# Kernel optimization log

Measured on AMD Instinct MI355X. Metric: run time of the kernel, lower is better.

The kernel has to match this reference:

```python
import jax, jax.numpy as jnp
import numpy as np

S, V, T = 128, 64, 128
N_RBF, CUTOFF = 16, 6.0
N_ATOM, N_PROT, N_FRAG, N_BATCH = 8192, 16384, 1024, 8
K, R, EPS = 32, 3.0, 1e-4
ES_DIM = N_RBF + S + S + T  # 400
HID = 256
GATE = S + 2 * V  # 256


def rbf_encode(d):
    mu = jnp.linspace(0.0, CUTOFF, N_RBF)
    gamma = N_RBF / CUTOFF
    return jnp.exp(-jnp.square(gamma * (d[..., None] - mu)))


def tp_conv(hs, hv, src, dst, diff, es, valid, n_dst, W1, b1, W2, b2, Ws, Wv):
    """Gather -> edge-scalar-gated tensor product -> scatter-add (EquivariantTPConv)."""
    w = jax.nn.silu(es @ W1 + b1) @ W2 + b2                      # [E, S+2V] edge gates
    unit = diff / (jnp.linalg.norm(diff, axis=-1, keepdims=True) + 1e-8)
    xs = hs[src] @ Ws                                            # [E, S]
    xv = jnp.einsum('evc,vw->ewc', hv[src], Wv)                  # [E, V, 3]
    ms = jnp.where(valid[:, None], w[:, :S] * xs, 0.0)
    mv = jnp.where(valid[:, None, None],
                   w[:, S:S + V, None] * xv + w[:, S + V:, None] * unit[:, None, :], 0.0)
    agg_s = jax.ops.segment_sum(ms, dst, num_segments=n_dst)
    agg_v = jax.ops.segment_sum(mv.reshape(-1, V * 3), dst, num_segments=n_dst).reshape(n_dst, V, 3)
    return agg_s, agg_v


def fragment_inertia(local_pos, fragment_id):
    r2 = jnp.sum(local_pos * local_pos, axis=-1)
    eye = jnp.eye(3, dtype=local_pos.dtype)
    I_atom = r2[:, None, None] * eye - local_pos[:, :, None] * local_pos[:, None, :]
    I_frag = jax.ops.segment_sum(I_atom.reshape(-1, 9), fragment_id, num_segments=N_FRAG).reshape(N_FRAG, 3, 3)
    trace = jnp.trace(I_frag, axis1=-2, axis2=-1)[:, None, None]
    return I_frag + EPS * jnp.maximum(trace, 1.0) * eye


def _forward(atom_pos, prot_pos, local_pos, h_atom_s, h_atom_v, h_prot_s, h_prot_v,
             h_frag_s, h_frag_v, t_emb_atom,
             W1_ra, b1_ra, W2_ra, b2_ra, Ws_ra, Wv_ra,
             W1_af, b1_af, W2_af, b2_af, Ws_af, Wv_af,
             Wo_s, Wo_v, Wf_s, Wf_v,
             fragment_id, atom_batch, prot_batch):
    # ---- bipartite radius graph prot -> atom via masked cdist + topk ----
    d2 = (jnp.sum(atom_pos * atom_pos, -1)[:, None]
          + jnp.sum(prot_pos * prot_pos, -1)[None, :]
          - 2.0 * atom_pos @ prot_pos.T)
    dist = jnp.sqrt(jnp.maximum(d2, 0.0))                        # [N_ATOM, N_PROT]
    mask = (dist <= R) & (atom_batch[:, None] == prot_batch[None, :])
    dinf = jnp.where(mask, dist, jnp.inf)
    neg_top, src = jax.lax.top_k(-dinf, K)                       # K nearest per atom
    valid = jnp.isfinite(neg_top).reshape(-1)
    src = src.reshape(-1)
    dst = jnp.repeat(jnp.arange(N_ATOM), K)
    # ---- residue->atom TP conv ----
    diff_ra = atom_pos[dst] - prot_pos[src]
    dist_ra = jnp.linalg.norm(diff_ra, axis=-1)
    ra_es = jnp.concatenate([rbf_encode(dist_ra), h_prot_s[src], h_atom_s[dst], t_emb_atom[dst]], -1)
    ms, mv = tp_conv(h_prot_s, h_prot_v, src, dst, diff_ra, ra_es, valid, N_ATOM,
                     W1_ra, b1_ra, W2_ra, b2_ra, Ws_ra, Wv_ra)
    ha_s = h_atom_s + jax.nn.silu(ms @ Wo_s)
    ha_v = h_atom_v + jnp.einsum('nvc,vw->nwc', mv, Wo_v)
    # ---- fragment centers + atom->frag re-lift TP conv ----
    ones = jnp.ones((N_ATOM,), atom_pos.dtype)
    cnt = jnp.maximum(jax.ops.segment_sum(ones, fragment_id, num_segments=N_FRAG), 1.0)
    T_frag = jax.ops.segment_sum(atom_pos, fragment_id, num_segments=N_FRAG) / cnt[:, None]
    r_af = atom_pos - T_frag[fragment_id]
    af_es = jnp.concatenate([rbf_encode(jnp.linalg.norm(r_af, axis=-1)), ha_s,
                             h_frag_s[fragment_id], t_emb_atom], -1)
    af_valid = jnp.ones((N_ATOM,), bool)
    fs, fv = tp_conv(ha_s, ha_v, jnp.arange(N_ATOM), fragment_id, r_af, af_es, af_valid, N_FRAG,
                     W1_af, b1_af, W2_af, b2_af, Ws_af, Wv_af)
    hf_s = h_frag_s + jax.nn.silu(fs @ Wf_s)
    hf_v = h_frag_v + jnp.einsum('nvc,vw->nwc', fv, Wf_v)
    I_frag = fragment_inertia(local_pos, fragment_id)
    # single packed output [N_ATOM, 2*(S+3V)+9]; frag quantities gathered per atom
    return jnp.concatenate([ha_s, ha_v.reshape(N_ATOM, -1),
                            hf_s[fragment_id], hf_v.reshape(N_FRAG, -1)[fragment_id],
                            I_frag.reshape(N_FRAG, 9)[fragment_id]], -1)


def setup_inputs() -> dict:
    key = jax.random.key(0)
    ks = jax.random.split(key, 32)
    def w(k, shape, fan_in):
        return jax.random.normal(k, shape, jnp.float32) / np.sqrt(fan_in).astype(np.float32)
    return dict(
        atom_pos=jax.random.normal(ks[0], (N_ATOM, 3), jnp.float32),
        prot_pos=jax.random.normal(ks[1], (N_PROT, 3), jnp.float32),
        local_pos=jax.random.normal(ks[2], (N_ATOM, 3), jnp.float32),
        h_atom_s=jax.random.normal(ks[3], (N_ATOM, S), jnp.float32),
        h_atom_v=jax.random.normal(ks[4], (N_ATOM, V, 3), jnp.float32),
        h_prot_s=jax.random.normal(ks[5], (N_PROT, S), jnp.float32),
        h_prot_v=jax.random.normal(ks[6], (N_PROT, V, 3), jnp.float32),
        h_frag_s=jax.random.normal(ks[7], (N_FRAG, S), jnp.float32),
        h_frag_v=jax.random.normal(ks[8], (N_FRAG, V, 3), jnp.float32),
        t_emb_atom=jax.random.normal(ks[9], (N_ATOM, T), jnp.float32),
        W1_ra=w(ks[10], (ES_DIM, HID), ES_DIM), b1_ra=jnp.zeros((HID,), jnp.float32),
        W2_ra=w(ks[11], (HID, GATE), HID), b2_ra=jnp.zeros((GATE,), jnp.float32),
        Ws_ra=w(ks[12], (S, S), S), Wv_ra=w(ks[13], (V, V), V),
        W1_af=w(ks[14], (ES_DIM, HID), ES_DIM), b1_af=jnp.zeros((HID,), jnp.float32),
        W2_af=w(ks[15], (HID, GATE), HID), b2_af=jnp.zeros((GATE,), jnp.float32),
        Ws_af=w(ks[16], (S, S), S), Wv_af=w(ks[17], (V, V), V),
        Wo_s=w(ks[18], (S, S), S), Wo_v=w(ks[19], (V, V), V),
        Wf_s=w(ks[20], (S, S), S), Wf_v=w(ks[21], (V, V), V),
        fragment_id=jax.random.randint(ks[22], (N_ATOM,), 0, N_FRAG),
        atom_batch=jnp.sort(jax.random.randint(ks[23], (N_ATOM,), 0, N_BATCH)),
        prot_batch=jnp.sort(jax.random.randint(ks[24], (N_PROT,), 0, N_BATCH)),
    )


def reference(atom_pos, prot_pos, local_pos, h_atom_s, h_atom_v, h_prot_s, h_prot_v,
              h_frag_s, h_frag_v, t_emb_atom,
              W1_ra, b1_ra, W2_ra, b2_ra, Ws_ra, Wv_ra,
              W1_af, b1_af, W2_af, b2_af, Ws_af, Wv_af,
              Wo_s, Wo_v, Wf_s, Wf_v,
              fragment_id, atom_batch, prot_batch):
    return _forward(atom_pos, prot_pos, local_pos, h_atom_s, h_atom_v, h_prot_s, h_prot_v,
                    h_frag_s, h_frag_v, t_emb_atom,
                    W1_ra, b1_ra, W2_ra, b2_ra, Ws_ra, Wv_ra,
                    W1_af, b1_af, W2_af, b2_af, Ws_af, Wv_af,
                    Wo_s, Wo_v, Wf_s, Wf_v,
                    fragment_id, atom_batch, prot_batch)
```

## Files before the change

kernel.cpp:

```cpp
#include <hip/hip_runtime.h>
#include <hip/hip_bf16.h>

#define N_ATOM 8192
#define N_PROT 16384
#define N_FRAG 1024
#define KNN    32
#define OUTC   649

typedef __attribute__((ext_vector_type(8))) short bf16x8;
typedef __attribute__((ext_vector_type(4))) float f32x4;

__device__ __forceinline__ float silu_f(float x){ return x / (1.f + __expf(-x)); }
__device__ __forceinline__ unsigned long long ullmin2(unsigned long long a, unsigned long long b){ return a < b ? a : b; }

__device__ __forceinline__ short f2bf(float x){
    __hip_bfloat16 h = __float2bfloat16(x);
    return *reinterpret_cast<short*>(&h);
}
__device__ __forceinline__ unsigned f2bf2(float lo, float hi){
    __hip_bfloat162 h2;
    h2.x = __float2bfloat16(lo);
    h2.y = __float2bfloat16(hi);
    return *reinterpret_cast<unsigned*>(&h2);
}
__device__ __forceinline__ float bf2f(short s){
    return __uint_as_float(((unsigned)(unsigned short)s) << 16);
}

__global__ void k_ranges(const int* __restrict__ pbatch, int* __restrict__ pstart){
    int b = threadIdx.x;
    if (b <= 8){
        int lo = 0, hi = N_PROT;
        while (lo < hi){ int mid = (lo + hi) >> 1; if (pbatch[mid] < b) lo = mid + 1; else hi = mid; }
        pstart[b] = lo;
    }
}

__global__ __launch_bounds__(256) void k_knn(const float* __restrict__ apos,
                                             const float* __restrict__ ppos,
                                             const int* __restrict__ abatch,
                                             const int* __restrict__ pstart,
                                             int* __restrict__ src_out){
    __shared__ int h1[256];
    __shared__ int s_info[4];
    __shared__ int s_nsel;
    __shared__ int s_nbound;
    __shared__ unsigned long long s_bound[512];

    const int i = blockIdx.x, t = threadIdx.x;
    const int lane = t & 63;
    const int b = abatch[i];
    const int p0 = pstart[b], p1 = pstart[b+1];
    const float ax = apos[i*3+0], ay = apos[i*3+1], az = apos[i*3+2];
    const float a2 = ax*ax + ay*ay + az*az;
    const float BINSCALE = 256.0f / 9.0f;

    unsigned kb[12];
    int jj[12];
    int bn[12];
#pragma unroll
    for (int q = 0; q < 12; ++q){
        int j = p0 + q*256 + t;
        unsigned kk = 0xFFFFFFFFu;
        int bin = -1;
        if (j < p1){
            float px = ppos[j*3+0], py = ppos[j*3+1], pz = ppos[j*3+2];
            float p2 = px*px + py*py + pz*pz;
            float dt = ax*px + ay*py + az*pz;
            float d2 = fmaxf((a2 + p2) - 2.0f*dt, 0.f);
            if (d2 <= 9.0f){
                kk = __float_as_uint(d2);
                bin = (int)(d2 * BINSCALE);
                if (bin > 255) bin = 255;
            }
        }
        kb[q] = kk; jj[q] = j; bn[q] = bin;
    }
    h1[t] = 0;
    if (t == 0){ s_nsel = 0; s_nbound = 0; }
    __syncthreads();
#pragma unroll
    for (int q = 0; q < 12; ++q)
        if (bn[q] >= 0) atomicAdd(&h1[bn[q]], 1);
    __syncthreads();
    if (t < 64){
        int base = t*4;
        int a0 = h1[base], a1 = h1[base+1], a2i = h1[base+2], a3 = h1[base+3];
        int lsum = a0 + a1 + a2i + a3;
        int sc = lsum;
#pragma unroll
        for (int off = 1; off < 64; off <<= 1){
            int v = __shfl_up(sc, off);
            if (lane >= off) sc += v;
        }
        int ex = sc - lsum;
        h1[base]   = ex + a0;
        h1[base+1] = ex + a0 + a1;
        h1[base+2] = ex + a0 + a1 + a2i;
        h1[base+3] = sc;
        if (t == 63) s_info[3] = sc;
    }
    __syncthreads();
    const int total = s_info[3];
    const int kth = (total < KNN) ? total : KNN;
    if (kth > 0){
        int cum  = h1[t];
        int prev = (t == 0) ? 0 : h1[t-1];
        if (cum >= kth && prev < kth){ s_info[0] = t; }
    }
    __syncthreads();
    const int B = s_info[0];
    if (kth > 0){
#pragma unroll
        for (int q = 0; q < 12; ++q){
            if (bn[q] < 0) continue;
            if (bn[q] < B){
                int pos = atomicAdd(&s_nsel, 1);
                src_out[i*KNN + pos] = jj[q];
            } else if (bn[q] == B){
                int bi = atomicAdd(&s_nbound, 1);
                if (bi < 512) s_bound[bi] = ((unsigned long long)kb[q] << 32) | (unsigned)jj[q];
            }
        }
    }
    __syncthreads();
    const int base_n = s_nsel;
    const int R = kth - base_n;
    if (t < 64 && R > 0){
        int L = s_nbound; if (L > 512) L = 512;
        for (int r = 0; r < R; ++r){
            unsigned long long m = ~0ull;
            for (int idx = lane; idx < L; idx += 64) m = ullmin2(m, s_bound[idx]);
#pragma unroll
            for (int off = 32; off >= 1; off >>= 1)
                m = ullmin2(m, (unsigned long long)__shfl_xor((unsigned long long)m, off));
            if (lane == 0) src_out[i*KNN + base_n + r] = (int)(unsigned)(m & 0xFFFFFFFFull);
            for (int idx = lane; idx < L; idx += 64)
                if (s_bound[idx] == m) s_bound[idx] = ~0ull;
        }
    }
    if (t < KNN && t >= kth) src_out[i*KNN + t] = -1;
}

__global__ void k_fragsum(const float* __restrict__ apos, const float* __restrict__ lpos,
                          const int* __restrict__ fid,
                          float* __restrict__ cnt, float* __restrict__ tsum, float* __restrict__ isum){
    int a = blockIdx.x*256 + threadIdx.x;
    if (a >= N_ATOM) return;
    int f = fid[a];
    atomicAdd(&cnt[f], 1.f);
    atomicAdd(&tsum[f*3+0], apos[a*3+0]);
    atomicAdd(&tsum[f*3+1], apos[a*3+1]);
    atomicAdd(&tsum[f*3+2], apos[a*3+2]);
    float x = lpos[a*3+0], y = lpos[a*3+1], z = lpos[a*3+2];
    float r2 = x*x + y*y + z*z;
    atomicAdd(&isum[f*9+0], r2 - x*x);
    atomicAdd(&isum[f*9+1], -(x*y));
    atomicAdd(&isum[f*9+2], -(x*z));
    atomicAdd(&isum[f*9+3], -(y*x));
    atomicAdd(&isum[f*9+4], r2 - y*y);
    atomicAdd(&isum[f*9+5], -(y*z));
    atomicAdd(&isum[f*9+6], -(z*x));
    atomicAdd(&isum[f*9+7], -(z*y));
    atomicAdd(&isum[f*9+8], r2 - z*z);
}

__global__ void k_fragcent(const float* __restrict__ cnt, const float* __restrict__ tsum,
                           const float* __restrict__ isum,
                           float* __restrict__ tfrag, float* __restrict__ ifin){
    int f = blockIdx.x*256 + threadIdx.x;
    if (f >= N_FRAG) return;
    float cn = fmaxf(cnt[f], 1.f);
    tfrag[f*3+0] = tsum[f*3+0] / cn;
    tfrag[f*3+1] = tsum[f*3+1] / cn;
    tfrag[f*3+2] = tsum[f*3+2] / cn;
    float tr  = isum[f*9+0] + isum[f*9+4] + isum[f*9+8];
    float add = 1e-4f * fmaxf(tr, 1.f);
#pragma unroll
    for (int q = 0; q < 9; ++q){
        float v = isum[f*9+q];
        if (q == 0 || q == 4 || q == 8) v += add;
        ifin[f*9+q] = v;
    }
}

__global__ __launch_bounds__(1024) void k_csr_prefix(const float* __restrict__ cnt,
                                                     int* __restrict__ csr_off,
                                                     int* __restrict__ csr_cur){
    __shared__ int s[1024];
    int t = threadIdx.x;
    int v = (int)cnt[t];
    s[t] = v;
    __syncthreads();
    for (int off = 1; off < 1024; off <<= 1){
        int x = (t >= off) ? s[t-off] : 0;
        __syncthreads();
        s[t] += x;
        __syncthreads();
    }
    int incl = s[t];
    int excl = incl - v;
    csr_off[t] = excl;
    csr_cur[t] = excl;
    if (t == 1023) csr_off[1024] = incl;
}

__global__ void k_csr_scatter(const int* __restrict__ fid, int* __restrict__ csr_cur,
                              int* __restrict__ csr_atom){
    int a = blockIdx.x*256 + threadIdx.x;
    if (a >= N_ATOM) return;
    int f = fid[a];
    int pos = atomicAdd(&csr_cur[f], 1);
    csr_atom[pos] = a;
}

__global__ void k_pack(const float* __restrict__ W1, const float* __restrict__ W2,
                       const float* __restrict__ Ws, const float* __restrict__ Wv,
                       const float* __restrict__ W1a, const float* __restrict__ W2a,
                       const float* __restrict__ Wsa, const float* __restrict__ Wva,
                       const float* __restrict__ Wos, const float* __restrict__ Wov,
                       short* __restrict__ W1p, short* __restrict__ W2p,
                       short* __restrict__ Wsp, short* __restrict__ Wvp,
                       short* __restrict__ W1cp,
                       short* __restrict__ W1ap, short* __restrict__ W2ap,
                       short* __restrict__ Wsap, short* __restrict__ Wvap,
                       short* __restrict__ Wosp, short* __restrict__ Wovp){
    int id = blockIdx.x*256 + threadIdx.x;
    if (id < 5120){
        int kt = id/1024, rem = id%1024, nt = rem/64, l = rem%64;
#pragma unroll
        for (int jj = 0; jj < 8; ++jj){
            int k = kt*32 + ((l>>4)<<3) + jj, n = nt*16 + (l&15);
            W1p[(size_t)id*8 + jj] = (k < 144) ? f2bf(W1[(size_t)k*256 + n]) : (short)0;
        }
    } else if (id < 13312){
        int id2 = id - 5120;
        int kt = id2/1024, rem = id2%1024, nt = rem/64, l = rem%64;
#pragma unroll
        for (int jj = 0; jj < 8; ++jj){
            int k = kt*32 + ((l>>4)<<3) + jj, n = nt*16 + (l&15);
            W2p[(size_t)id2*8 + jj] = f2bf(W2[(size_t)k*256 + n]);
        }
    } else if (id < 15360){
        int id2 = id - 13312;
        int kt = id2/512, rem = id2%512, nt = rem/64, l = rem%64;
#pragma unroll
        for (int jj = 0; jj < 8; ++jj){
            int k = kt*32 + ((l>>4)<<3) + jj, n = nt*16 + (l&15);
            Wsp[(size_t)id2*8 + jj] = f2bf(Ws[(size_t)k*128 + n]);
        }
    } else if (id < 15872){
        int id2 = id - 15360;
        int kt = id2/256, rem = id2%256, nt = rem/64, l = rem%64;
#pragma unroll
        for (int jj = 0; jj < 8; ++jj){
            int k = kt*32 + ((l>>4)<<3) + jj, n = nt*16 + (l&15);
            Wvp[(size_t)id2*8 + jj] = f2bf(Wv[(size_t)k*64 + n]);
        }
    } else if (id < 24064){
        int id2 = id - 15872;
        int kt = id2/1024, rem = id2%1024, nt = rem/64, l = rem%64;
#pragma unroll
        for (int jj = 0; jj < 8; ++jj){
            int k = kt*32 + ((l>>4)<<3) + jj, n = nt*16 + (l&15);
            W1cp[(size_t)id2*8 + jj] = f2bf(W1[(size_t)(144 + k)*256 + n]);
        }
    } else if (id < 37376){
        int id2 = id - 24064;
        int kt = id2/1024, rem = id2%1024, nt = rem/64, l = rem%64;
#pragma unroll
        for (int jj = 0; jj < 8; ++jj){
            int k = kt*32 + ((l>>4)<<3) + jj, n = nt*16 + (l&15);
            W1ap[(size_t)id2*8 + jj] = (k < 400) ? f2bf(W1a[(size_t)k*256 + n]) : (short)0;
        }
    } else if (id < 45568){
        int id2 = id - 37376;
        int kt = id2/1024, rem = id2%1024, nt = rem/64, l = rem%64;
#pragma unroll
        for (int jj = 0; jj < 8; ++jj){
            int k = kt*32 + ((l>>4)<<3) + jj, n = nt*16 + (l&15);
            W2ap[(size_t)id2*8 + jj] = f2bf(W2a[(size_t)k*256 + n]);
        }
    } else if (id < 47616){
        int id2 = id - 45568;
        int kt = id2/512, rem = id2%512, nt = rem/64, l = rem%64;
#pragma unroll
        for (int jj = 0; jj < 8; ++jj){
            int k = kt*32 + ((l>>4)<<3) + jj, n = nt*16 + (l&15);
            Wsap[(size_t)id2*8 + jj] = f2bf(Wsa[(size_t)k*128 + n]);
        }
    } else if (id < 48128){
        int id2 = id - 47616;
        int kt = id2/256, rem = id2%256, nt = rem/64, l = rem%64;
#pragma unroll
        for (int jj = 0; jj < 8; ++jj){
            int k = kt*32 + ((l>>4)<<3) + jj, n = nt*16 + (l&15);
            Wvap[(size_t)id2*8 + jj] = f2bf(Wva[(size_t)k*64 + n]);
        }
    } else if (id < 50176){
        int id2 = id - 48128;
        int kt = id2/512, rem = id2%512, nt = rem/64, l = rem%64;
#pragma unroll
        for (int jj = 0; jj < 8; ++jj){
            int k = kt*32 + ((l>>4)<<3) + jj, n = nt*16 + (l&15);
            Wosp[(size_t)id2*8 + jj] = f2bf(Wos[(size_t)k*128 + n]);
        }
    } else if (id < 50688){
        int id2 = id - 50176;
        int kt = id2/256, rem = id2%256, nt = rem/64, l = rem%64;
#pragma unroll
        for (int jj = 0; jj < 8; ++jj){
            int k = kt*32 + ((l>>4)<<3) + jj, n = nt*16 + (l&15);
            Wovp[(size_t)id2*8 + jj] = f2bf(Wov[(size_t)k*64 + n]);
        }
    }
}

__global__ __launch_bounds__(256) void k_ctx(const float* __restrict__ has_,
                                             const float* __restrict__ temb,
                                             const short* __restrict__ W1cp,
                                             const float* __restrict__ b1,
                                             float* __restrict__ common){
    __shared__ __align__(16) char s_a[64*512];
    const int t = threadIdx.x, l = t & 63, w = t >> 6, g = l >> 4;
    const int a0 = blockIdx.x * 64;
    {
        int r = t & 63, seg = t >> 6;
        const float* srcp = (seg < 2) ? (has_ + (size_t)(a0 + r)*128 + seg*64)
                                      : (temb + (size_t)(a0 + r)*128 + (seg - 2)*64);
#pragma unroll
        for (int q = 0; q < 16; ++q){
            float4 x = *(const float4*)(srcp + q*4);
            int col = seg*64 + q*4;
            int off = (r*512 + col*2) ^ ((r & 7) << 4);
            *(unsigned*)(s_a + off)     = f2bf2(x.x, x.y);
            *(unsigned*)(s_a + off + 4) = f2bf2(x.z, x.w);
        }
    }
    __syncthreads();
    f32x4 acc[4][4];
#pragma unroll
    for (int mt = 0; mt < 4; ++mt)
#pragma unroll
        for (int nt = 0; nt < 4; ++nt) acc[mt][nt] = (f32x4){0.f,0.f,0.f,0.f};
    for (int ks = 0; ks < 8; ++ks){
        bf16x8 afr[4];
#pragma unroll
        for (int mt = 0; mt < 4; ++mt){
            int row = mt*16 + (l & 15);
            int off = (row*512 + ks*64 + g*16) ^ ((row & 7) << 4);
            afr[mt] = *(const bf16x8*)(s_a + off);
        }
#pragma unroll
        for (int nt = 0; nt < 4; ++nt){
            bf16x8 b = *(const bf16x8*)(W1cp + ((size_t)((ks*16 + (w*4 + nt))*64 + l))*8);
#pragma unroll
            for (int mt = 0; mt < 4; ++mt)
                acc[mt][nt] = __builtin_amdgcn_mfma_f32_16x16x32_bf16(afr[mt], b, acc[mt][nt], 0, 0, 0);
        }
    }
#pragma unroll
    for (int nt = 0; nt < 4; ++nt){
        int col = w*64 + nt*16 + (l & 15);
        float bb = b1[col];
#pragma unroll
        for (int mt = 0; mt < 4; ++mt)
#pragma unroll
            for (int r = 0; r < 4; ++r){
                int row = mt*16 + g*4 + r;
                common[(size_t)(a0 + row)*256 + col] = acc[mt][nt][r] + bb;
            }
    }
}

#define ES_STR 336
__global__ __launch_bounds__(512, 2) void k_ra3(
    const float* __restrict__ apos, const float* __restrict__ ppos,
    const float* __restrict__ hps,  const float* __restrict__ hpv,
    const short* __restrict__ W1p, const short* __restrict__ W2p,
    const short* __restrict__ Wsp, const short* __restrict__ Wvp,
    const float* __restrict__ common, const float* __restrict__ b2,
    const int* __restrict__ src,
    short* __restrict__ msR, short* __restrict__ mvR)
{
    __shared__ __align__(16) char s_es[32*ES_STR];
    __shared__ __align__(16) char s_h1[32*512];
    __shared__ __align__(16) char s_hpv[3*4096];
    __shared__ float s_unit[32][3];

    const int t = threadIdx.x;
    const int i = blockIdx.x;
    const int l = t & 63, w = t >> 6, g = l >> 4, r0 = l & 15;
    const int xm = (r0 & 7) << 4;
    float* s_mvA = (float*)s_es;
    float* s_mvB = s_mvA + 192;

    {
        const int e = t >> 4, sub = t & 15;
        const int j = src[i*KNN + e];
        float dx = 0.f, dy = 0.f, dz = 0.f, dist = 0.f;
        if (j >= 0){
            dx = apos[i*3+0] - ppos[j*3+0];
            dy = apos[i*3+1] - ppos[j*3+1];
            dz = apos[i*3+2] - ppos[j*3+2];
            dist = sqrtf(dx*dx + dy*dy + dz*dz);
        }
        if (sub == 0){
            float inv = 1.f / (dist + 1e-8f);
            s_unit[e][0] = dx*inv; s_unit[e][1] = dy*inv; s_unit[e][2] = dz*inv;
        }
        if (sub < 2){
            const float gamma = 16.0f / 6.0f;
#pragma unroll
            for (int q = 0; q < 4; ++q){
                int kk = sub*8 + q*2;
                float mu0  = 0.4f * (float)kk;
                float mu1  = 0.4f * (float)(kk+1);
                float a0 = gamma * (dist - mu0);
                float a1 = gamma * (dist - mu1);
                float e0 = (j >= 0) ? __expf(-(a0*a0)) : 0.f;
                float e1 = (j >= 0) ? __expf(-(a1*a1)) : 0.f;
                *(unsigned*)(s_es + e*ES_STR + kk*2) = f2bf2(e0, e1);
            }
        }
        if (sub < 8) *(int*)(s_es + e*ES_STR + 288 + sub*4) = 0;
#pragma unroll
        for (int q = 0; q < 2; ++q){
            float4 x = (j >= 0) ? *(const float4*)(hps + (size_t)j*128 + sub*8 + q*4)
                                : make_float4(0.f,0.f,0.f,0.f);
            *(unsigned*)(s_es + e*ES_STR + 32 + sub*16 + q*8)     = f2bf2(x.x, x.y);
            *(unsigned*)(s_es + e*ES_STR + 32 + sub*16 + q*8 + 4) = f2bf2(x.z, x.w);
        }
        const int em = (e & 7) << 4;
#pragma unroll
        for (int q = 0; q < 3; ++q){
            float4 x = (j >= 0) ? *(const float4*)(hpv + (size_t)j*192 + sub*12 + q*4)
                                : make_float4(0.f,0.f,0.f,0.f);
            float xv4[4] = {x.x, x.y, x.z, x.w};
#pragma unroll
            for (int m = 0; m < 4; ++m){
                int idx = sub*12 + q*4 + m;
                int v = idx/3, c = idx - v*3;
                *(short*)(s_hpv + c*4096 + e*128 + ((v*2) ^ em)) = f2bf(xv4[m]);
            }
        }
    }
    __syncthreads();

    f32x4 acc1[2][2];
#pragma unroll
    for (int mt = 0; mt < 2; ++mt)
#pragma unroll
        for (int nt = 0; nt < 2; ++nt) acc1[mt][nt] = (f32x4){0.f,0.f,0.f,0.f};
    for (int ks = 0; ks < 5; ++ks){
        bf16x8 a0 = *(const bf16x8*)(s_es + r0*ES_STR + ks*64 + g*16);
        bf16x8 a1 = *(const bf16x8*)(s_es + (16 + r0)*ES_STR + ks*64 + g*16);
#pragma unroll
        for (int nt = 0; nt < 2; ++nt){
            bf16x8 b = *(const bf16x8*)(W1p + ((size_t)((ks*16 + (w*2 + nt))*64 + l))*8);
            acc1[0][nt] = __builtin_amdgcn_mfma_f32_16x16x32_bf16(a0, b, acc1[0][nt], 0, 0, 0);
            acc1[1][nt] = __builtin_amdgcn_mfma_f32_16x16x32_bf16(a1, b, acc1[1][nt], 0, 0, 0);
        }
    }

#pragma unroll
    for (int nt = 0; nt < 2; ++nt){
        int col = w*32 + nt*16 + r0;
        float cm = common[(size_t)i*256 + col];
#pragma unroll
        for (int mt = 0; mt < 2; ++mt)
#pragma unroll
            for (int r = 0; r < 4; ++r){
                float v = silu_f(acc1[mt][nt][r] + cm);
                int row = mt*16 + g*4 + r;
                int off = (row*512 + col*2) ^ ((row & 7) << 4);
                *(short*)(s_h1 + off) = f2bf(v);
            }
    }

    f32x4 accxs[2][2];
#pragma unroll
    for (int mt = 0; mt < 2; ++mt)
#pragma unroll
        for (int nt = 0; nt < 2; ++nt) accxs[mt][nt] = (f32x4){0.f,0.f,0.f,0.f};
    if (w < 4){
        for (int ks = 0; ks < 4; ++ks){
            bf16x8 a0 = *(const bf16x8*)(s_es + r0*ES_STR + 32 + ks*64 + g*16);
            bf16x8 a1 = *(const bf16x8*)(s_es + (16 + r0)*ES_STR + 32 + ks*64 + g*16);
#pragma unroll
            for (int nt = 0; nt < 2; ++nt){
                bf16x8 b = *(const bf16x8*)(Wsp + ((size_t)((ks*8 + (w*2 + nt))*64 + l))*8);
                accxs[0][nt] = __builtin_amdgcn_mfma_f32_16x16x32_bf16(a0, b, accxs[0][nt], 0, 0, 0);
                accxs[1][nt] = __builtin_amdgcn_mfma_f32_16x16x32_bf16(a1, b, accxs[1][nt], 0, 0, 0);
            }
        }
    }
    __syncthreads();

    f32x4 accw[2][2];
#pragma unroll
    for (int mt = 0; mt < 2; ++mt)
#pragma unroll
        for (int nt = 0; nt < 2; ++nt) accw[mt][nt] = (f32x4){0.f,0.f,0.f,0.f};
    for (int ks = 0; ks < 8; ++ks){
        int off0 = (r0*512 + ks*64 + g*16) ^ xm;
        bf16x8 a0 = *(const bf16x8*)(s_h1 + off0);
        bf16x8 a1 = *(const bf16x8*)(s_h1 + off0 + 8192);
#pragma unroll
        for (int nt = 0; nt < 2; ++nt){
            bf16x8 b = *(const bf16x8*)(W2p + ((size_t)((ks*16 + (w*2 + nt))*64 + l))*8);
            accw[0][nt] = __builtin_amdgcn_mfma_f32_16x16x32_bf16(a0, b, accw[0][nt], 0, 0, 0);
            accw[1][nt] = __builtin_amdgcn_mfma_f32_16x16x32_bf16(a1, b, accw[1][nt], 0, 0, 0);
        }
    }
    float b2v[2];
#pragma unroll
    for (int nt = 0; nt < 2; ++nt) b2v[nt] = b2[w*32 + nt*16 + r0];

    if (w < 4){
#pragma unroll
        for (int nt = 0; nt < 2; ++nt){
            float p = 0.f;
#pragma unroll
            for (int mt = 0; mt < 2; ++mt)
#pragma unroll
                for (int r = 0; r < 4; ++r)
                    p = fmaf(accw[mt][nt][r] + b2v[nt], accxs[mt][nt][r], p);
            p += __shfl_xor(p, 16);
            p += __shfl_xor(p, 32);
            if (l < 16) msR[(size_t)i*128 + w*32 + nt*16 + r0] = f2bf(p);
        }
    } else if (w < 6){
        bf16x8 bv[2][2];
#pragma unroll
        for (int ks = 0; ks < 2; ++ks)
#pragma unroll
            for (int nt = 0; nt < 2; ++nt)
                bv[ks][nt] = *(const bf16x8*)(Wvp + ((size_t)((ks*4 + (w-4)*2 + nt)*64 + l))*8);
#pragma unroll
        for (int c = 0; c < 3; ++c){
            f32x4 accxv[2][2];
#pragma unroll
            for (int mt = 0; mt < 2; ++mt)
#pragma unroll
                for (int nt = 0; nt < 2; ++nt) accxv[mt][nt] = (f32x4){0.f,0.f,0.f,0.f};
#pragma unroll
            for (int ks = 0; ks < 2; ++ks){
                int off0 = c*4096 + r0*128 + ((ks*64 + g*16) ^ xm);
                bf16x8 a0 = *(const bf16x8*)(s_hpv + off0);
                bf16x8 a1 = *(const bf16x8*)(s_hpv + off0 + 2048);
#pragma unroll
                for (int nt = 0; nt < 2; ++nt){
                    accxv[0][nt] = __builtin_amdgcn_mfma_f32_16x16x32_bf16(a0, bv[ks][nt], accxv[0][nt], 0, 0, 0);
                    accxv[1][nt] = __builtin_amdgcn_mfma_f32_16x16x32_bf16(a1, bv[ks][nt], accxv[1][nt], 0, 0, 0);
                }
            }
#pragma unroll
            for (int nt = 0; nt < 2; ++nt){
                float p = 0.f;
#pragma unroll
                for (int mt = 0; mt < 2; ++mt)
#pragma unroll
                    for (int r = 0; r < 4; ++r)
                        p = fmaf(accw[mt][nt][r] + b2v[nt], accxv[mt][nt][r], p);
                p += __shfl_xor(p, 16);
                p += __shfl_xor(p, 32);
                if (l < 16) s_mvA[c*64 + (w-4)*32 + nt*16 + r0] = p;
            }
        }
    } else {
        float uu[8][3];
#pragma unroll
        for (int mt = 0; mt < 2; ++mt)
#pragma unroll
            for (int r = 0; r < 4; ++r){
                int e = mt*16 + g*4 + r;
#pragma unroll
                for (int c = 0; c < 3; ++c) uu[mt*4+r][c] = s_unit[e][c];
            }
#pragma unroll
        for (int c = 0; c < 3; ++c)
#pragma unroll
            for (int nt = 0; nt < 2; ++nt){
                float p = 0.f;
#pragma unroll
                for (int mt = 0; mt < 2; ++mt)
#pragma unroll
                    for (int r = 0; r < 4; ++r)
                        p = fmaf(accw[mt][nt][r] + b2v[nt], uu[mt*4+r][c], p);
                p += __shfl_xor(p, 16);
                p += __shfl_xor(p, 32);
                if (l < 16) s_mvB[c*64 + (w-6)*32 + nt*16 + r0] = p;
            }
    }
    __syncthreads();

    if (t < 192){
        int wi = t & 63, cc = t >> 6;
        float v = s_mvA[cc*64 + wi] + s_mvB[cc*64 + wi];
        mvR[((size_t)i*3 + cc)*64 + wi] = f2bf(v);
    }
}

__global__ __launch_bounds__(256) void k_ra_out(
    const short* __restrict__ msR, const short* __restrict__ mvR,
    const short* __restrict__ Wosp, const short* __restrict__ Wovp,
    const float* __restrict__ has_, const float* __restrict__ hav,
    float* __restrict__ out)
{
    const int t = threadIdx.x, l = t & 63, w = t >> 6, g = l >> 4, r0 = l & 15;
    const int a0 = blockIdx.x * 32;

    f32x4 acc[2][2];
#pragma unroll
    for (int mt = 0; mt < 2; ++mt)
#pragma unroll
        for (int nt = 0; nt < 2; ++nt) acc[mt][nt] = (f32x4){0.f,0.f,0.f,0.f};
    for (int ks = 0; ks < 4; ++ks){
        bf16x8 af0 = *(const bf16x8*)(msR + ((size_t)(a0 + r0)*128 + ks*32 + g*8));
        bf16x8 af1 = *(const bf16x8*)(msR + ((size_t)(a0 + 16 + r0)*128 + ks*32 + g*8));
#pragma unroll
        for (int nt = 0; nt < 2; ++nt){
            bf16x8 b = *(const bf16x8*)(Wosp + ((size_t)((ks*8 + (w*2 + nt))*64 + l))*8);
            acc[0][nt] = __builtin_amdgcn_mfma_f32_16x16x32_bf16(af0, b, acc[0][nt], 0, 0, 0);
            acc[1][nt] = __builtin_amdgcn_mfma_f32_16x16x32_bf16(af1, b, acc[1][nt], 0, 0, 0);
        }
    }
#pragma unroll
    for (int nt = 0; nt < 2; ++nt){
        int col = w*32 + nt*16 + r0;
#pragma unroll
        for (int mt = 0; mt < 2; ++mt)
#pragma unroll
            for (int r = 0; r < 4; ++r){
                int a = a0 + mt*16 + g*4 + r;
                out[(size_t)a*OUTC + col] = has_[(size_t)a*128 + col] + silu_f(acc[mt][nt][r]);
            }
    }

    f32x4 accv[6];
#pragma unroll
    for (int mt = 0; mt < 6; ++mt) accv[mt] = (f32x4){0.f,0.f,0.f,0.f};
    for (int ks = 0; ks < 2; ++ks){
        bf16x8 b = *(const bf16x8*)(Wovp + ((size_t)((ks*4 + w)*64 + l))*8);
#pragma unroll
        for (int mt = 0; mt < 6; ++mt){
            bf16x8 af = *(const bf16x8*)(mvR + ((size_t)(a0*3 + mt*16 + r0)*64 + ks*32 + g*8));
            accv[mt] = __builtin_amdgcn_mfma_f32_16x16x32_bf16(af, b, accv[mt], 0, 0, 0);
        }
    }
    const int wi = w*16 + r0;
#pragma unroll
    for (int mt = 0; mt < 6; ++mt)
#pragma unroll
        for (int r = 0; r < 4; ++r){
            int R = mt*16 + g*4 + r;
            int a = a0 + R/3, c = R - (R/3)*3;
            out[(size_t)a*OUTC + 128 + wi*3 + c] = hav[(size_t)a*192 + wi*3 + c] + accv[mt][r];
        }
}

#define AES_STR 848
__global__ __launch_bounds__(256, 2) void k_af2(
    const float* __restrict__ apos, const float* __restrict__ tfrag,
    const float* __restrict__ hfs_in, const float* __restrict__ temb,
    const short* __restrict__ W1p, const float* __restrict__ b1,
    const short* __restrict__ W2p, const float* __restrict__ b2,
    const short* __restrict__ Wsp, const short* __restrict__ Wvp,
    const int* __restrict__ fragid, const float* __restrict__ out,
    short* __restrict__ msA, short* __restrict__ mvA)
{
    __shared__ __align__(16) char s_es[16*AES_STR];
    __shared__ __align__(16) char s_h1[16*512];
    __shared__ __align__(16) char s_pv[3*2048];
    __shared__ float s_unit[16][3];
    float* s_upr = (float*)s_es;

    const int t = threadIdx.x, a0 = blockIdx.x*16;
    const int l = t & 63, w = t >> 6, g = l >> 4, r0 = l & 15;
    const int xm = (r0 & 7) << 4;

    {
        const int e = t >> 4, sub = t & 15;
        const int a = a0 + e;
        const int f = fragid[a];
        float rx = apos[a*3+0] - tfrag[f*3+0];
        float ry = apos[a*3+1] - tfrag[f*3+1];
        float rz = apos[a*3+2] - tfrag[f*3+2];
        float dist = sqrtf(rx*rx + ry*ry + rz*rz);
        if (sub == 0){
            float inv = 1.f / (dist + 1e-8f);
            s_unit[e][0] = rx*inv; s_unit[e][1] = ry*inv; s_unit[e][2] = rz*inv;
        }
        if (sub < 2){
            const float gamma = 16.0f / 6.0f;
#pragma unroll
            for (int q = 0; q < 4; ++q){
                int kk = sub*8 + q*2;
                float mu0  = 0.4f * (float)kk;
                float mu1  = 0.4f * (float)(kk+1);
                float a0f = gamma * (dist - mu0);
                float a1f = gamma * (dist - mu1);
                *(unsigned*)(s_es + e*AES_STR + kk*2) = f2bf2(__expf(-(a0f*a0f)), __expf(-(a1f*a1f)));
            }
        }
#pragma unroll
        for (int q = 0; q < 4; ++q){
            float v0 = out[(size_t)a*OUTC + sub*8 + q*2];
            float v1 = out[(size_t)a*OUTC + sub*8 + q*2 + 1];
            *(unsigned*)(s_es + e*AES_STR + 32 + (sub*8 + q*2)*2) = f2bf2(v0, v1);
        }
#pragma unroll
        for (int q = 0; q < 2; ++q){
            float4 x = *(const float4*)(hfs_in + (size_t)f*128 + sub*8 + q*4);
            *(unsigned*)(s_es + e*AES_STR + 288 + sub*16 + q*8)     = f2bf2(x.x, x.y);
            *(unsigned*)(s_es + e*AES_STR + 288 + sub*16 + q*8 + 4) = f2bf2(x.z, x.w);
        }
#pragma unroll
        for (int q = 0; q < 2; ++q){
            float4 x = *(const float4*)(temb + (size_t)a*128 + sub*8 + q*4);
            *(unsigned*)(s_es + e*AES_STR + 544 + sub*16 + q*8)     = f2bf2(x.x, x.y);
            *(unsigned*)(s_es + e*AES_STR + 544 + sub*16 + q*8 + 4) = f2bf2(x.z, x.w);
        }
        *(short*)(s_es + e*AES_STR + 800 + sub*2) = 0;
        const int em = (e & 7) << 4;
#pragma unroll
        for (int q = 0; q < 12; ++q){
            int idx = sub*12 + q;
            float v = out[(size_t)a*OUTC + 128 + idx];
            int vv = idx/3, c = idx - vv*3;
            *(short*)(s_pv + c*2048 + e*128 + ((vv*2) ^ em)) = f2bf(v);
        }
    }
    __syncthreads();

    f32x4 acc1[4];
#pragma unroll
    for (int nt = 0; nt < 4; ++nt) acc1[nt] = (f32x4){0.f,0.f,0.f,0.f};
    for (int ks = 0; ks < 13; ++ks){
        bf16x8 a0f = *(const bf16x8*)(s_es + r0*AES_STR + ks*64 + g*16);
#pragma unroll
        for (int nt = 0; nt < 4; ++nt){
            bf16x8 b = *(const bf16x8*)(W1p + ((size_t)((ks*16 + (w*4 + nt))*64 + l))*8);
            acc1[nt] = __builtin_amdgcn_mfma_f32_16x16x32_bf16(a0f, b, acc1[nt], 0, 0, 0);
        }
    }
#pragma unroll
    for (int nt = 0; nt < 4; ++nt){
        int col = w*64 + nt*16 + r0;
        float bb = b1[col];
#pragma unroll
        for (int r = 0; r < 4; ++r){
            float v = silu_f(acc1[nt][r] + bb);
            int row = g*4 + r;
            int off = (row*512 + col*2) ^ ((row & 7) << 4);
            *(short*)(s_h1 + off) = f2bf(v);
        }
    }
    f32x4 accxs[4];
#pragma unroll
    for (int nt = 0; nt < 4; ++nt) accxs[nt] = (f32x4){0.f,0.f,0.f,0.f};
    if (w < 2){
        for (int ks = 0; ks < 4; ++ks){
            bf16x8 a0f = *(const bf16x8*)(s_es + r0*AES_STR + 32 + ks*64 + g*16);
#pragma unroll
            for (int nt = 0; nt < 4; ++nt){
                bf16x8 b = *(const bf16x8*)(Wsp + ((size_t)((ks*8 + (w*4 + nt))*64 + l))*8);
                accxs[nt] = __builtin_amdgcn_mfma_f32_16x16x32_bf16(a0f, b, accxs[nt], 0, 0, 0);
            }
        }
    }
    __syncthreads();

    f32x4 accw[4];
#pragma unroll
    for (int nt = 0; nt < 4; ++nt) accw[nt] = (f32x4){0.f,0.f,0.f,0.f};
    for (int ks = 0; ks < 8; ++ks){
        int off0 = (r0*512 + ks*64 + g*16) ^ xm;
        bf16x8 a0f = *(const bf16x8*)(s_h1 + off0);
#pragma unroll
        for (int nt = 0; nt < 4; ++nt){
            bf16x8 b = *(const bf16x8*)(W2p + ((size_t)((ks*16 + (w*4 + nt))*64 + l))*8);
            accw[nt] = __builtin_amdgcn_mfma_f32_16x16x32_bf16(a0f, b, accw[nt], 0, 0, 0);
        }
    }
    float b2v[4];
#pragma unroll
    for (int nt = 0; nt < 4; ++nt) b2v[nt] = b2[w*64 + nt*16 + r0];

    if (w == 3){
        float uu[4][3];
#pragma unroll
        for (int r = 0; r < 4; ++r){
            int e = g*4 + r;
#pragma unroll
            for (int c = 0; c < 3; ++c) uu[r][c] = s_unit[e][c];
        }
#pragma unroll
        for (int nt = 0; nt < 4; ++nt){
            int wi = nt*16 + r0;
#pragma unroll
            for (int r = 0; r < 4; ++r){
                int e = g*4 + r;
                float gate = accw[nt][r] + b2v[nt];
#pragma unroll
                for (int c = 0; c < 3; ++c)
                    s_upr[e*192 + wi*3 + c] = gate * uu[r][c];
            }
        }
    }
    __syncthreads();

    if (w < 2){
#pragma unroll
        for (int nt = 0; nt < 4; ++nt){
            int col = w*64 + nt*16 + r0;
#pragma unroll
            for (int r = 0; r < 4; ++r){
                int e = g*4 + r;
                float p = (accw[nt][r] + b2v[nt]) * accxs[nt][r];
                msA[(size_t)(a0 + e)*128 + col] = f2bf(p);
            }
        }
    } else if (w == 2){
        bf16x8 bv[2][4];
#pragma unroll
        for (int ks = 0; ks < 2; ++ks)
#pragma unroll
            for (int nt = 0; nt < 4; ++nt)
                bv[ks][nt] = *(const bf16x8*)(Wvp + ((size_t)((ks*4 + nt)*64 + l))*8);
#pragma unroll
        for (int c = 0; c < 3; ++c){
            f32x4 accxv[4];
#pragma unroll
            for (int nt = 0; nt < 4; ++nt) accxv[nt] = (f32x4){0.f,0.f,0.f,0.f};
#pragma unroll
            for (int ks = 0; ks < 2; ++ks){
                int off0 = c*2048 + r0*128 + ((ks*64 + g*16) ^ xm);
                bf16x8 a0f = *(const bf16x8*)(s_pv + off0);
#pragma unroll
                for (int nt = 0; nt < 4; ++nt)
                    accxv[nt] = __builtin_amdgcn_mfma_f32_16x16x32_bf16(a0f, bv[ks][nt], accxv[nt], 0, 0, 0);
            }
#pragma unroll
            for (int nt = 0; nt < 4; ++nt){
                int wi = nt*16 + r0;
#pragma unroll
                for (int r = 0; r < 4; ++r){
                    int e = g*4 + r;
                    float p = (accw[nt][r] + b2v[nt]) * accxv[nt][r]
                            + s_upr[e*192 + wi*3 + c];
                    mvA[(size_t)(a0 + e)*192 + wi*3 + c] = f2bf(p);
                }
            }
        }
    }
}

__global__ __launch_bounds__(256) void k_fragupd(
    const int* __restrict__ csr_off, const int* __restrict__ csr_atom,
    const short* __restrict__ msA, const short* __restrict__ mvA,
    const float* __restrict__ hfs_in, const float* __restrict__ hfv_in,
    const float* __restrict__ Wfs, const float* __restrict__ Wfv,
    const float* __restrict__ ifin,
    float* __restrict__ out)
{
    __shared__ __align__(16) float s_fs[128];
    __shared__ __align__(16) float s_fv[192];
    const int f = blockIdx.x, t = threadIdx.x;
    const int n0 = csr_off[f], n1 = csr_off[f+1];
    if (t < 128){
        float s = 0.f;
        for (int n = n0; n < n1; ++n){
            int a = csr_atom[n];
            s += bf2f(msA[(size_t)a*128 + t]);
        }
        s_fs[t] = s;
    }
    if (t >= 64){
        int idx = t - 64;
        float s = 0.f;
        for (int n = n0; n < n1; ++n){
            int a = csr_atom[n];
            s += bf2f(mvA[(size_t)a*192 + idx]);
        }
        s_fv[(idx % 3)*64 + (idx / 3)] = s;
    }
    __syncthreads();
    if (t < 128){
        float o = 0.f;
        for (int k = 0; k < 128; k += 4){
            const float* wr = &Wfs[k*128 + t];
            float4 m4 = *(const float4*)&s_fs[k];
            o = fmaf(m4.x, wr[0],   o);
            o = fmaf(m4.y, wr[128], o);
            o = fmaf(m4.z, wr[256], o);
            o = fmaf(m4.w, wr[384], o);
        }
        float val = hfs_in[f*128 + t] + silu_f(o);
        for (int n = n0; n < n1; ++n)
            out[(size_t)csr_atom[n]*OUTC + 320 + t] = val;
    }
    if (t < 192){
        const int wi = t & 63, cc = t >> 6;
        float o = 0.f;
        for (int v = 0; v < 64; v += 4){
            const float* wr = &Wfv[v*64 + wi];
            float4 m4 = *(const float4*)&s_fv[cc*64 + v];
            o = fmaf(m4.x, wr[0],   o);
            o = fmaf(m4.y, wr[64],  o);
            o = fmaf(m4.z, wr[128], o);
            o = fmaf(m4.w, wr[192], o);
        }
        float val = hfv_in[f*192 + wi*3 + cc] + o;
        for (int n = n0; n < n1; ++n)
            out[(size_t)csr_atom[n]*OUTC + 448 + wi*3 + cc] = val;
    } else if (t < 201){
        int q = t - 192;
        float val = ifin[f*9 + q];
        for (int n = n0; n < n1; ++n)
            out[(size_t)csr_atom[n]*OUTC + 640 + q] = val;
    }
}

extern "C" void kernel_launch(void* const* d_in, const int* in_sizes, int n_in,
                              void* d_out, int out_size, void* d_ws, size_t ws_size,
                              hipStream_t stream)
{
    const float* atom_pos   = (const float*)d_in[0];
    const float* prot_pos   = (const float*)d_in[1];
    const float* local_pos  = (const float*)d_in[2];
    const float* h_atom_s   = (const float*)d_in[3];
    const float* h_atom_v   = (const float*)d_in[4];
    const float* h_prot_s   = (const float*)d_in[5];
    const float* h_prot_v   = (const float*)d_in[6];
    const float* h_frag_s   = (const float*)d_in[7];
    const float* h_frag_v   = (const float*)d_in[8];
    const float* t_emb      = (const float*)d_in[9];
    const float* W1_ra = (const float*)d_in[10]; const float* b1_ra = (const float*)d_in[11];
    const float* W2_ra = (const float*)d_in[12]; const float* b2_ra = (const float*)d_in[13];
    const float* Ws_ra = (const float*)d_in[14]; const float* Wv_ra = (const float*)d_in[15];
    const float* W1_af = (const float*)d_in[16]; const float* b1_af = (const float*)d_in[17];
    const float* W2_af = (const float*)d_in[18]; const float* b2_af = (const float*)d_in[19];
    const float* Ws_af = (const float*)d_in[20]; const float* Wv_af = (const float*)d_in[21];
    const float* Wo_s  = (const float*)d_in[22]; const float* Wo_v  = (const float*)d_in[23];
    const float* Wf_s  = (const float*)d_in[24]; const float* Wf_v  = (const float*)d_in[25];
    const int* fragment_id = (const int*)d_in[26];
    const int* atom_batch  = (const int*)d_in[27];
    const int* prot_batch  = (const int*)d_in[28];
    float* out = (float*)d_out;

    float* cnt   = (float*)d_ws;
    float* tsum  = cnt  + 1024;
    float* isum  = tsum + 3072;
    float* tfrag = isum + 9216;
    float* ifin  = tfrag + 3072;
    float* hfs   = ifin + 9216;
    float* hfv   = hfs  + 1024*128;
    int*   pstart   = (int*)(hfv + 1024*192);
    int*   src      = pstart + 16;
    int*   csr_off  = src + N_ATOM*KNN;
    int*   csr_cur  = csr_off + 1025;
    int*   csr_atom = csr_cur + 1024;
    uintptr_t pal = ((uintptr_t)(csr_atom + 8192) + 127) & ~(uintptr_t)127;
    float* common = (float*)pal;
    short* msA = (short*)common;
    short* mvA = msA + (size_t)8192*128;
    short* W1p  = (short*)(common + (size_t)8192*256);
    short* W2p  = W1p  + 40960;
    short* Wsp  = W2p  + 65536;
    short* Wvp  = Wsp  + 16384;
    short* W1cp = Wvp  + 4096;
    short* W1ap = W1cp + 65536;
    short* W2ap = W1ap + 106496;
    short* Wsap = W2ap + 65536;
    short* Wvap = Wsap + 16384;
    short* Wosp = Wvap + 4096;
    short* Wovp = Wosp + 16384;
    short* msR  = Wovp + 4096;
    short* mvR  = msR + (size_t)8192*128;

    size_t zero_bytes = (size_t)(1024 + 3072 + 9216) * sizeof(float);
    hipMemsetAsync(cnt, 0, zero_bytes, stream);

    k_pack    <<<198, 256, 0, stream>>>(W1_ra, W2_ra, Ws_ra, Wv_ra, W1_af, W2_af, Ws_af, Wv_af,
                                        Wo_s, Wo_v,
                                        W1p, W2p, Wsp, Wvp, W1cp, W1ap, W2ap, Wsap, Wvap,
                                        Wosp, Wovp);
    k_ranges  <<<1, 64, 0, stream>>>(prot_batch, pstart);
    k_knn     <<<N_ATOM, 256, 0, stream>>>(atom_pos, prot_pos, atom_batch, pstart, src);
    k_ctx     <<<N_ATOM/64, 256, 0, stream>>>(h_atom_s, t_emb, W1cp, b1_ra, common);
    k_fragsum <<<N_ATOM/256, 256, 0, stream>>>(atom_pos, local_pos, fragment_id, cnt, tsum, isum);
    k_fragcent<<<N_FRAG/256, 256, 0, stream>>>(cnt, tsum, isum, tfrag, ifin);
    k_csr_prefix<<<1, 1024, 0, stream>>>(cnt, csr_off, csr_cur);
    k_csr_scatter<<<N_ATOM/256, 256, 0, stream>>>(fragment_id, csr_cur, csr_atom);
    k_ra3     <<<N_ATOM, 512, 0, stream>>>(atom_pos, prot_pos, h_prot_s, h_prot_v,
                                           W1p, W2p, Wsp, Wvp, common, b2_ra,
                                           src, msR, mvR);
    k_ra_out  <<<N_ATOM/32, 256, 0, stream>>>(msR, mvR, Wosp, Wovp, h_atom_s, h_atom_v, out);
    k_af2     <<<N_ATOM/16, 256, 0, stream>>>(atom_pos, tfrag, h_frag_s, t_emb,
                                              W1ap, b1_af, W2ap, b2_af, Wsap, Wvap,
                                              fragment_id, out, msA, mvA);
    k_fragupd <<<N_FRAG, 256, 0, stream>>>(csr_off, csr_atom, msA, mvA,
                                           h_frag_s, h_frag_v, Wf_s, Wf_v, ifin, out);
}
```

Baseline: 252.6 us.

## Pre-convert protein features to bf16 and fold fragcent into CSR prefix kernel

Adds a conversion kernel that turns protein scalar features into bf16 and protein vector features into a channel-major bf16 layout once, instead of converting them for every gathered edge. The radius-graph message kernel then gathers 16-byte bf16 vectors straight into shared memory, which halves gather bytes and removes per-element conversion and scattered short stores. The fragment centroid/inertia finalization is merged into the single-block prefix kernel to save a launch. This costs an extra pass over all protein features and some scratch memory.

```diff
diff --git a/kernel.cpp b/kernel.cpp
--- a/kernel.cpp
+++ b/kernel.cpp
@@ -33,6 +33,33 @@
         int lo = 0, hi = N_PROT;
         while (lo < hi){ int mid = (lo + hi) >> 1; if (pbatch[mid] < b) lo = mid + 1; else hi = mid; }
         pstart[b] = lo;
+    }
+}
+
+__global__ __launch_bounds__(256) void k_cvt(const float* __restrict__ hps,
+                                             const float* __restrict__ hpv,
+                                             short* __restrict__ hpsB,
+                                             short* __restrict__ hpvT){
+    int id = blockIdx.x*256 + threadIdx.x;
+    if (id < N_PROT*16){
+        const float* s = hps + (size_t)id*8;
+        float4 x0 = *(const float4*)(s);
+        float4 x1 = *(const float4*)(s+4);
+        unsigned* d = (unsigned*)(hpsB + (size_t)id*8);
+        d[0] = f2bf2(x0.x, x0.y); d[1] = f2bf2(x0.z, x0.w);
+        d[2] = f2bf2(x1.x, x1.y); d[3] = f2bf2(x1.z, x1.w);
+    } else {
+        int id2 = id - N_PROT*16;
+        if (id2 < N_PROT*24){
+            int j = id2 / 24, r = id2 % 24;
+            short tmp[8];
+#pragma unroll
+            for (int u = 0; u < 8; ++u){
+                int o = r*8 + u, c = o >> 6, v = o & 63;
+                tmp[u] = f2bf(hpv[(size_t)j*192 + v*3 + c]);
+            }
+            *(bf16x8*)(hpvT + (size_t)j*192 + r*8) = *(bf16x8*)tmp;
+        }
     }
 }
 
@@ -165,32 +192,32 @@
     atomicAdd(&isum[f*9+8], r2 - z*z);
 }
 
-__global__ void k_fragcent(const float* __restrict__ cnt, const float* __restrict__ tsum,
-                           const float* __restrict__ isum,
-                           float* __restrict__ tfrag, float* __restrict__ ifin){
-    int f = blockIdx.x*256 + threadIdx.x;
-    if (f >= N_FRAG) return;
-    float cn = fmaxf(cnt[f], 1.f);
-    tfrag[f*3+0] = tsum[f*3+0] / cn;
-    tfrag[f*3+1] = tsum[f*3+1] / cn;
-    tfrag[f*3+2] = tsum[f*3+2] / cn;
-    float tr  = isum[f*9+0] + isum[f*9+4] + isum[f*9+8];
-    float add = 1e-4f * fmaxf(tr, 1.f);
-#pragma unroll
-    for (int q = 0; q < 9; ++q){
-        float v = isum[f*9+q];
-        if (q == 0 || q == 4 || q == 8) v += add;
-        ifin[f*9+q] = v;
-    }
-}
-
 __global__ __launch_bounds__(1024) void k_csr_prefix(const float* __restrict__ cnt,
+                                                     const float* __restrict__ tsum,
+                                                     const float* __restrict__ isum,
                                                      int* __restrict__ csr_off,
-                                                     int* __restrict__ csr_cur){
+                                                     int* __restrict__ csr_cur,
+                                                     float* __restrict__ tfrag,
+                                                     float* __restrict__ ifin){
     __shared__ int s[1024];
     int t = threadIdx.x;
-    int v = (int)cnt[t];
+    float cn_raw = cnt[t];
+    int v = (int)cn_raw;
     s[t] = v;
+    {
+        float cn = fmaxf(cn_raw, 1.f);
+        tfrag[t*3+0] = tsum[t*3+0] / cn;
+        tfrag[t*3+1] = tsum[t*3+1] / cn;
+        tfrag[t*3+2] = tsum[t*3+2] / cn;
+        float tr  = isum[t*9+0] + isum[t*9+4] + isum[t*9+8];
+        float add = 1e-4f * fmaxf(tr, 1.f);
+#pragma unroll
+        for (int q = 0; q < 9; ++q){
+            float vv = isum[t*9+q];
+            if (q == 0 || q == 4 || q == 8) vv += add;
+            ifin[t*9+q] = vv;
+        }
+    }
     __syncthreads();
     for (int off = 1; off < 1024; off <<= 1){
         int x = (t >= off) ? s[t-off] : 0;
@@ -376,7 +403,7 @@
 #define ES_STR 336
 __global__ __launch_bounds__(512, 2) void k_ra3(
     const float* __restrict__ apos, const float* __restrict__ ppos,
-    const float* __restrict__ hps,  const float* __restrict__ hpv,
+    const short* __restrict__ hpsB, const short* __restrict__ hpvT,
     const short* __restrict__ W1p, const short* __restrict__ W2p,
     const short* __restrict__ Wsp, const short* __restrict__ Wvp,
     const float* __restrict__ common, const float* __restrict__ b2,
@@ -424,24 +451,18 @@
             }
         }
         if (sub < 8) *(int*)(s_es + e*ES_STR + 288 + sub*4) = 0;
-#pragma unroll
-        for (int q = 0; q < 2; ++q){
-            float4 x = (j >= 0) ? *(const float4*)(hps + (size_t)j*128 + sub*8 + q*4)
-                                : make_float4(0.f,0.f,0.f,0.f);
-            *(unsigned*)(s_es + e*ES_STR + 32 + sub*16 + q*8)     = f2bf2(x.x, x.y);
-            *(unsigned*)(s_es + e*ES_STR + 32 + sub*16 + q*8 + 4) = f2bf2(x.z, x.w);
+        const bf16x8 zv = (bf16x8){0,0,0,0,0,0,0,0};
+        {
+            bf16x8 hc = (j >= 0) ? *(const bf16x8*)(hpsB + (size_t)j*128 + sub*8) : zv;
+            *(bf16x8*)(s_es + e*ES_STR + 32 + sub*16) = hc;
         }
         const int em = (e & 7) << 4;
-#pragma unroll
-        for (int q = 0; q < 3; ++q){
-            float4 x = (j >= 0) ? *(const float4*)(hpv + (size_t)j*192 + sub*12 + q*4)
-                                : make_float4(0.f,0.f,0.f,0.f);
-            float xv4[4] = {x.x, x.y, x.z, x.w};
-#pragma unroll
-            for (int m = 0; m < 4; ++m){
-                int idx = sub*12 + q*4 + m;
-                int v = idx/3, c = idx - v*3;
-                *(short*)(s_hpv + c*4096 + e*128 + ((v*2) ^ em)) = f2bf(xv4[m]);
+        {
+            bf16x8 c0 = (j >= 0) ? *(const bf16x8*)(hpvT + (size_t)j*192 + sub*8) : zv;
+            *(bf16x8*)(s_hpv + (sub>>3)*4096 + e*128 + (((sub&7)<<4) ^ em)) = c0;
+            if (sub < 8){
+                bf16x8 c1 = (j >= 0) ? *(const bf16x8*)(hpvT + (size_t)j*192 + (16+sub)*8) : zv;
+                *(bf16x8*)(s_hpv + 2*4096 + e*128 + ((sub<<4) ^ em)) = c1;
             }
         }
     }
@@ -979,6 +1000,8 @@
     short* Wovp = Wosp + 16384;
     short* msR  = Wovp + 4096;
     short* mvR  = msR + (size_t)8192*128;
+    short* hpsB = mvR + (size_t)8192*192;
+    short* hpvT = hpsB + (size_t)N_PROT*128;
 
     size_t zero_bytes = (size_t)(1024 + 3072 + 9216) * sizeof(float);
     hipMemsetAsync(cnt, 0, zero_bytes, stream);
@@ -987,14 +1010,14 @@
                                         Wo_s, Wo_v,
                                         W1p, W2p, Wsp, Wvp, W1cp, W1ap, W2ap, Wsap, Wvap,
                                         Wosp, Wovp);
+    k_cvt     <<<(N_PROT*16 + N_PROT*24)/256, 256, 0, stream>>>(h_prot_s, h_prot_v, hpsB, hpvT);
     k_ranges  <<<1, 64, 0, stream>>>(prot_batch, pstart);
     k_knn     <<<N_ATOM, 256, 0, stream>>>(atom_pos, prot_pos, atom_batch, pstart, src);
     k_ctx     <<<N_ATOM/64, 256, 0, stream>>>(h_atom_s, t_emb, W1cp, b1_ra, common);
     k_fragsum <<<N_ATOM/256, 256, 0, stream>>>(atom_pos, local_pos, fragment_id, cnt, tsum, isum);
-    k_fragcent<<<N_FRAG/256, 256, 0, stream>>>(cnt, tsum, isum, tfrag, ifin);
-    k_csr_prefix<<<1, 1024, 0, stream>>>(cnt, csr_off, csr_cur);
+    k_csr_prefix<<<1, 1024, 0, stream>>>(cnt, tsum, isum, csr_off, csr_cur, tfrag, ifin);
     k_csr_scatter<<<N_ATOM/256, 256, 0, stream>>>(fragment_id, csr_cur, csr_atom);
-    k_ra3     <<<N_ATOM, 512, 0, stream>>>(atom_pos, prot_pos, h_prot_s, h_prot_v,
+    k_ra3     <<<N_ATOM, 512, 0, stream>>>(atom_pos, prot_pos, hpsB, hpvT,
                                            W1p, W2p, Wsp, Wvp, common, b2_ra,
                                            src, msR, mvR);
     k_ra_out  <<<N_ATOM/32, 256, 0, stream>>>(msR, mvR, Wosp, Wovp, h_atom_s, h_atom_v, out);
```

Result: faster. 244.1 us (-3.3%).
